# Kernel optimization log

Measured on AMD Instinct MI355X. Metric: run time of the kernel, lower is better.

Reference implementation:

```python
import jax, jax.numpy as jnp
import numpy as np

B, T, D = 4, 2048, 1024
RANK, FACTOR, SUB = 8, 64, 4
S = 4 * SUB  # 16


def construct_hamilton(A):
    # A: [rank, 4, sub, sub] -> [rank, 4*sub, 4*sub]
    r, i, j, k = A[:, 0], A[:, 1], A[:, 2], A[:, 3]
    return jnp.concatenate([
        jnp.concatenate([r, -i, -j, -k], axis=2),
        jnp.concatenate([i, r, -k, j], axis=2),
        jnp.concatenate([j, k, r, -i], axis=2),
        jnp.concatenate([k, -j, i, r], axis=2),
    ], axis=1)


def setup_inputs() -> dict:
    key = jax.random.key(0)
    k1, k2, k3 = jax.random.split(key, 3)
    x = jax.random.normal(k1, (B, T, D), dtype=jnp.float32)
    A = jax.random.normal(k2, (RANK, 4, SUB, SUB), dtype=jnp.float32)
    # orthogonal-ish init with (r+1)^-0.5 scaling, like the torch init
    fB = jax.random.normal(k3, (RANK, FACTOR, FACTOR), dtype=jnp.float32)
    q, _ = jnp.linalg.qr(fB)
    scale = (jnp.arange(RANK, dtype=jnp.float32) + 1.0) ** -0.5
    factors_B = q * scale[:, None, None]
    bias = jnp.zeros((D,), dtype=jnp.float32)
    return {"x": x, "A": A, "factors_B": factors_B, "bias": bias}


def reference(x, A, factors_B, bias):
    Bb, Tt, Dd = x.shape
    x_flat = x.reshape(-1, S, FACTOR)          # [N, s, i]
    H = construct_hamilton(A)                   # [r, k, s]
    wav = jnp.einsum('nsi,rji->rnsj', x_flat, factors_B)  # [r, N, s, j]
    out = jnp.einsum('rnsj,rks->nkj', wav, H)   # [N, k, j]
    return out.reshape(Bb, Tt, Dd) + bias
```

## Files before the change

kernel.cpp:

```cpp
#include <hip/hip_runtime.h>
#include <stdint.h>

#define RANKS 8
#define MDIM 8192
#define KDIM 1024
#define NDIM 1024
#define BM 128
#define BN 128
#define BK 32
#define NT (KDIM / BK)
#define THREADS 256

typedef __bf16 bf16x8 __attribute__((ext_vector_type(8)));
typedef float f32x4 __attribute__((ext_vector_type(4)));

__device__ __forceinline__ unsigned short f2bf(float f) {
  union { float f; uint32_t u; } v; v.f = f;
  uint32_t u = v.u;
  u += 0x7FFFu + ((u >> 16) & 1u);
  return (unsigned short)(u >> 16);
}

__constant__ int   c_comp[4][4] = {{0,1,2,3},{1,0,3,2},{2,3,0,1},{3,2,1,0}};
__constant__ float c_sign[4][4] = {{1.f,-1.f,-1.f,-1.f},
                                   {1.f, 1.f,-1.f, 1.f},
                                   {1.f, 1.f, 1.f,-1.f},
                                   {1.f,-1.f, 1.f, 1.f}};

__global__ void build_W(const float* __restrict__ A, const float* __restrict__ fB,
                        unsigned short* __restrict__ W) {
  int idx = blockIdx.x * 256 + threadIdx.x;
  int p  = idx >> 8;
  int q4 = (idx & 255) << 2;
  int k = p >> 6, j = p & 63;
  int kb = k >> 2, ks = k & 3;
  int s = q4 >> 6;
  int sb = s >> 2, ss = s & 3;
  int   comp = c_comp[kb][sb];
  float sgn  = c_sign[kb][sb];
  float o0 = 0.f, o1 = 0.f, o2 = 0.f, o3 = 0.f;
  int i0 = q4 & 63;
#pragma unroll
  for (int r = 0; r < RANKS; ++r) {
    float h = sgn * A[r * 64 + comp * 16 + ks * 4 + ss];
    const float* fb = fB + r * 4096 + j * 64 + i0;
    o0 += h * fb[0]; o1 += h * fb[1]; o2 += h * fb[2]; o3 += h * fb[3];
  }
  ushort4 st;
  st.x = f2bf(o0); st.y = f2bf(o1); st.z = f2bf(o2); st.w = f2bf(o3);
  *reinterpret_cast<ushort4*>(W + (size_t)p * KDIM + q4) = st;
}

__device__ __forceinline__ void gload16(const void* g, void* l) {
  __builtin_amdgcn_global_load_lds(
      (const __attribute__((address_space(1))) unsigned int*)(uintptr_t)g,
      (__attribute__((address_space(3))) unsigned int*)(uintptr_t)l,
      16, 0, 0);
}

__global__ __launch_bounds__(THREADS, 2) void gemm_ham(
    const float* __restrict__ x, const unsigned short* __restrict__ W,
    const float* __restrict__ bias, float* __restrict__ out) {
  __shared__ float          Asm_[3][BM * BK];
  __shared__ unsigned short Bsm_[3][BN * BK];

  const int tid  = threadIdx.x;
  const int lane = tid & 63;
  const int wid  = tid >> 6;
  const int wr   = wid >> 1;
  const int wc   = wid & 1;
  const int rb   = lane & 15;
  const int qtr  = lane >> 4;

  const int flat = blockIdx.x;
  const int xg = flat & 7, ig = flat >> 3;
  const int bx = xg * 8 + (ig >> 3);
  const int by = ig & 7;
  const int row0 = bx * BM;
  const int col0 = by * BN;

  f32x4 acc[4][4];
  f32x4 zero = {0.f, 0.f, 0.f, 0.f};
#pragma unroll
  for (int m = 0; m < 4; ++m)
#pragma unroll
    for (int n = 0; n < 4; ++n) acc[m][n] = zero;

  auto stageA = [&](int kt, int slot) {
#pragma unroll
    for (int g = 0; g < 4; ++g) {
      int id = g * 256 + tid;
      int r = id >> 3, ct = id & 7;
      gload16(x + (size_t)(row0 + r) * KDIM + kt * BK + ((ct ^ (r & 7)) << 2),
              &Asm_[slot][id * 4]);
    }
  };
  auto stageB = [&](int kt, int slot) {
#pragma unroll
    for (int g = 0; g < 2; ++g) {
      int id = g * 256 + tid;
      int r = id >> 2, ct = id & 3;
      gload16(W + (size_t)(col0 + r) * KDIM + kt * BK + (ct << 3),
              &Bsm_[slot][id * 8]);
    }
  };

  stageA(0, 0); stageB(0, 0);
  stageA(1, 1); stageB(1, 1);
  asm volatile("s_waitcnt vmcnt(6)" ::: "memory");
  __builtin_amdgcn_sched_barrier(0);
  __builtin_amdgcn_s_barrier();
  __builtin_amdgcn_sched_barrier(0);

  int sc = 0;
#pragma unroll 1
  for (int t = 0; t < NT; ++t) {
    int s2 = sc + 2; if (s2 >= 3) s2 -= 3;
    if (t + 2 < NT) { stageA(t + 2, s2); stageB(t + 2, s2); }

    const char* Ab = reinterpret_cast<const char*>(&Asm_[sc][0]);
    const char* Bb = reinterpret_cast<const char*>(&Bsm_[sc][0]);
    bf16x8 af[4], bfr[4];
#pragma unroll
    for (int m = 0; m < 4; ++m) {
      int r = wr * 64 + m * 16 + rb;
      int u0 = (qtr * 2)     ^ (r & 7);
      int u1 = (qtr * 2 + 1) ^ (r & 7);
      f32x4 lo = *reinterpret_cast<const f32x4*>(Ab + r * 128 + (u0 << 4));
      f32x4 hi = *reinterpret_cast<const f32x4*>(Ab + r * 128 + (u1 << 4));
      bf16x8 v;
      v[0] = (__bf16)lo[0]; v[1] = (__bf16)lo[1]; v[2] = (__bf16)lo[2]; v[3] = (__bf16)lo[3];
      v[4] = (__bf16)hi[0]; v[5] = (__bf16)hi[1]; v[6] = (__bf16)hi[2]; v[7] = (__bf16)hi[3];
      af[m] = v;
    }
#pragma unroll
    for (int n = 0; n < 4; ++n) {
      int r = wc * 64 + n * 16 + rb;
      bfr[n] = *reinterpret_cast<const bf16x8*>(Bb + r * 64 + qtr * 16);
    }

    __builtin_amdgcn_s_setprio(1);
#pragma unroll
    for (int m = 0; m < 4; ++m)
#pragma unroll
      for (int n = 0; n < 4; ++n)
        acc[m][n] = __builtin_amdgcn_mfma_f32_16x16x32_bf16(af[m], bfr[n], acc[m][n], 0, 0, 0);
    __builtin_amdgcn_s_setprio(0);

    if (t < NT - 1) {
      if (t < NT - 2) asm volatile("s_waitcnt vmcnt(6)" ::: "memory");
      else            asm volatile("s_waitcnt vmcnt(0)" ::: "memory");
      __builtin_amdgcn_sched_barrier(0);
      __builtin_amdgcn_s_barrier();
      __builtin_amdgcn_sched_barrier(0);
    }
    sc = sc + 1; if (sc >= 3) sc -= 3;
  }

  const int crow = row0 + wr * 64 + qtr * 4;
  const int ccol = col0 + wc * 64 + rb;
#pragma unroll
  for (int n = 0; n < 4; ++n) {
    int c = ccol + n * 16;
    float bv = bias[c];
#pragma unroll
    for (int m = 0; m < 4; ++m)
#pragma unroll
      for (int v = 0; v < 4; ++v)
        out[(size_t)(crow + m * 16 + v) * NDIM + c] = acc[m][n][v] + bv;
  }
}

__global__ void fallback_kernel(const float* __restrict__ x, const float* __restrict__ A,
                                const float* __restrict__ fB, const float* __restrict__ bias,
                                float* __restrict__ out) {
  __shared__ float xrow[1024];
  const int n = blockIdx.x;
  const int tid = threadIdx.x;
  for (int t = tid; t < 1024; t += 256) xrow[t] = x[(size_t)n * 1024 + t];
  __syncthreads();
  for (int pp = 0; pp < 4; ++pp) {
    int p = pp * 256 + tid;
    int k = p >> 6, j = p & 63;
    int kb = k >> 2, ks = k & 3;
    float accv = 0.f;
    for (int s = 0; s < 16; ++s) {
      int sb = s >> 2, ss = s & 3;
      int comp = c_comp[kb][sb];
      float sgn = c_sign[kb][sb];
      float hA[RANKS];
#pragma unroll
      for (int r = 0; r < RANKS; ++r) hA[r] = sgn * A[r * 64 + comp * 16 + ks * 4 + ss];
      for (int i = 0; i < 64; ++i) {
        float w = 0.f;
#pragma unroll
        for (int r = 0; r < RANKS; ++r) w += hA[r] * fB[r * 4096 + j * 64 + i];
        accv += xrow[s * 64 + i] * w;
      }
    }
    out[(size_t)n * 1024 + p] = accv + bias[p];
  }
}

extern "C" void kernel_launch(void* const* d_in, const int* in_sizes, int n_in,
                              void* d_out, int out_size, void* d_ws, size_t ws_size,
                              hipStream_t stream) {
  const float* x    = (const float*)d_in[0];
  const float* A    = (const float*)d_in[1];
  const float* fB   = (const float*)d_in[2];
  const float* bias = (const float*)d_in[3];
  float* out = (float*)d_out;

  const size_t needW = (size_t)NDIM * KDIM * sizeof(unsigned short);
  if (ws_size >= needW) {
    unsigned short* W = (unsigned short*)d_ws;
    build_W<<<dim3(1024), dim3(256), 0, stream>>>(A, fB, W);
    gemm_ham<<<dim3((MDIM / BM) * (NDIM / BN)), dim3(THREADS), 0, stream>>>(x, W, bias, out);
  } else {
    fallback_kernel<<<dim3(MDIM), dim3(256), 0, stream>>>(x, A, fB, bias, out);
  }
}
```

Measured before the change: 37.27 us.

## Switch GEMM to double-buffered LDS with swizzled B tile and higher occupancy

Result: slower. 38.17 us (+2.4%).

```diff
diff --git a/kernel.cpp b/kernel.cpp
--- a/kernel.cpp
+++ b/kernel.cpp
@@ -58,11 +58,11 @@
       16, 0, 0);
 }
 
-__global__ __launch_bounds__(THREADS, 2) void gemm_ham(
+__global__ __launch_bounds__(THREADS, 3) void gemm_ham(
     const float* __restrict__ x, const unsigned short* __restrict__ W,
     const float* __restrict__ bias, float* __restrict__ out) {
-  __shared__ float          Asm_[3][BM * BK];
-  __shared__ unsigned short Bsm_[3][BN * BK];
+  __shared__ float          Asm_[2][BM * BK];
+  __shared__ unsigned short Bsm_[2][BN * BK];
 
   const int tid  = threadIdx.x;
   const int lane = tid & 63;
@@ -100,26 +100,21 @@
     for (int g = 0; g < 2; ++g) {
       int id = g * 256 + tid;
       int r = id >> 2, ct = id & 3;
-      gload16(W + (size_t)(col0 + r) * KDIM + kt * BK + (ct << 3),
+      gload16(W + (size_t)(col0 + r) * KDIM + kt * BK + ((ct ^ ((r >> 1) & 3)) << 3),
               &Bsm_[slot][id * 8]);
     }
   };
 
   stageA(0, 0); stageB(0, 0);
-  stageA(1, 1); stageB(1, 1);
-  asm volatile("s_waitcnt vmcnt(6)" ::: "memory");
-  __builtin_amdgcn_sched_barrier(0);
-  __builtin_amdgcn_s_barrier();
-  __builtin_amdgcn_sched_barrier(0);
-
-  int sc = 0;
+  __syncthreads();
+
+  int cur = 0;
 #pragma unroll 1
   for (int t = 0; t < NT; ++t) {
-    int s2 = sc + 2; if (s2 >= 3) s2 -= 3;
-    if (t + 2 < NT) { stageA(t + 2, s2); stageB(t + 2, s2); }
-
-    const char* Ab = reinterpret_cast<const char*>(&Asm_[sc][0]);
-    const char* Bb = reinterpret_cast<const char*>(&Bsm_[sc][0]);
+    if (t + 1 < NT) { stageA(t + 1, cur ^ 1); stageB(t + 1, cur ^ 1); }
+
+    const char* Ab = reinterpret_cast<const char*>(&Asm_[cur][0]);
+    const char* Bb = reinterpret_cast<const char*>(&Bsm_[cur][0]);
     bf16x8 af[4], bfr[4];
 #pragma unroll
     for (int m = 0; m < 4; ++m) {
@@ -136,25 +131,18 @@
 #pragma unroll
     for (int n = 0; n < 4; ++n) {
       int r = wc * 64 + n * 16 + rb;
-      bfr[n] = *reinterpret_cast<const bf16x8*>(Bb + r * 64 + qtr * 16);
-    }
-
-    __builtin_amdgcn_s_setprio(1);
+      int u = qtr ^ ((r >> 1) & 3);
+      bfr[n] = *reinterpret_cast<const bf16x8*>(Bb + r * 64 + (u << 4));
+    }
+
 #pragma unroll
     for (int m = 0; m < 4; ++m)
 #pragma unroll
       for (int n = 0; n < 4; ++n)
         acc[m][n] = __builtin_amdgcn_mfma_f32_16x16x32_bf16(af[m], bfr[n], acc[m][n], 0, 0, 0);
-    __builtin_amdgcn_s_setprio(0);
-
-    if (t < NT - 1) {
-      if (t < NT - 2) asm volatile("s_waitcnt vmcnt(6)" ::: "memory");
-      else            asm volatile("s_waitcnt vmcnt(0)" ::: "memory");
-      __builtin_amdgcn_sched_barrier(0);
-      __builtin_amdgcn_s_barrier();
-      __builtin_amdgcn_sched_barrier(0);
-    }
-    sc = sc + 1; if (sc >= 3) sc -= 3;
+
+    __syncthreads();
+    cur ^= 1;
   }
 
   const int crow = row0 + wr * 64 + qtr * 4;
```
